# Performance work log

Hardware: AMD Instinct MI355X
Metric: run time of the kernel (lower is better)

## Reference

```python
import jax, jax.numpy as jnp
import numpy as np

B, N, IN_DIM, OUT_DIM, K = 64, 256, 512, 512, 8
DK = OUT_DIM // K  # per-kernel feature dim


def setup_inputs() -> dict:
    key = jax.random.key(0)
    k1, k2, k3, k4 = jax.random.split(key, 4)
    node_feats = jax.random.normal(k1, (B, N, IN_DIM), dtype=jnp.float32)
    adj = jax.random.uniform(k2, (B, K, N, N), dtype=jnp.float32)
    weight = jax.random.normal(k3, (IN_DIM, OUT_DIM), dtype=jnp.float32) * (1.0 / np.sqrt(IN_DIM))
    bias = jax.random.normal(k4, (OUT_DIM,), dtype=jnp.float32) * 0.01
    return {"node_feats": node_feats, "adj": adj, "weight": weight, "bias": bias}


def reference(node_feats, adj, weight, bias):
    # kernel linear + ReLU: (b, n, out_dim)
    h = jax.nn.relu(jnp.einsum('bni,io->bno', node_feats, weight) + bias)
    # split into kernel slots: (b, n, k, dk)
    h = h.reshape(B, N, K, DK)
    # graph.aggregate: per-kernel dense message passing over adjacency
    # out[b,n,k,d] = sum_m adj[b,k,n,m] * h[b,m,k,d]
    agg = jnp.einsum('bknm,bmkd->bnkd', adj, h)
    return agg.reshape(B, N, OUT_DIM)
```

## Files before the change

### kernel.cpp

```cpp
#include <hip/hip_runtime.h>
#include <hip/hip_bf16.h>


typedef __attribute__((ext_vector_type(8))) short short8;
typedef __attribute__((ext_vector_type(4))) float floatx4;

__device__ __forceinline__ unsigned short f2bf(float f) {
    union { float f; unsigned u; } v; v.f = f;
    unsigned r = v.u + 0x7FFFu + ((v.u >> 16) & 1u);
    return (unsigned short)(r >> 16);
}

__device__ __forceinline__ unsigned pk2bf(float a, float b) {
    union { __hip_bfloat162 h; unsigned u; } cv;
    cv.h = __float22bfloat162_rn(make_float2(a, b));
    return cv.u;
}

__global__ __launch_bounds__(256) void wt_kernel(const float* __restrict__ W,
                                                 unsigned short* __restrict__ Wt) {
    __shared__ unsigned short t_lds[64 * 66];
    const int tile = blockIdx.x;
    const int k0 = (tile >> 3) * 64;
    const int o0 = (tile & 7) * 64;
    const int t = threadIdx.x;
    const int c = t & 63;
    const int rb = t >> 6;
#pragma unroll
    for (int i = 0; i < 16; ++i) {
        int r = i * 4 + rb;
        t_lds[c * 66 + r] = f2bf(W[(size_t)(k0 + r) * 512 + o0 + c]);
    }
    __syncthreads();
#pragma unroll
    for (int i = 0; i < 16; ++i) {
        int o_r = i * 4 + rb;
        Wt[(size_t)(o0 + o_r) * 512 + k0 + c] = t_lds[o_r * 66 + c];
    }
}

__global__ __launch_bounds__(256) void gemm_relu_kernel(
    const float* __restrict__ X, const unsigned short* __restrict__ Wt,
    const float* __restrict__ bias, unsigned short* __restrict__ hT) {
    __shared__ unsigned short a_lds[128 * 40];
    __shared__ unsigned short b_lds[128 * 40];

    const int id = blockIdx.x;
    const int r8 = id & 7;
    const int yt = (id >> 3) & 3;
    const int q  = id >> 5;
    const int m_tile = r8 + 8 * q;
    const int m_base = m_tile * 128;
    const int o_base = yt * 128;

    const int tid = threadIdx.x;
    const int lane = tid & 63, wid = tid >> 6;
    const int wm = (wid & 1) * 64, wn = (wid >> 1) * 64;
    const int lrow = lane & 15, quad = lane >> 4;

    floatx4 acc[4][4];
    const floatx4 fzero = {0.f, 0.f, 0.f, 0.f};
#pragma unroll
    for (int i = 0; i < 4; ++i)
#pragma unroll
        for (int j = 0; j < 4; ++j) acc[i][j] = fzero;

    for (int kb = 0; kb < 16; ++kb) {
        const int k0 = kb * 32;
#pragma unroll
        for (int i = 0; i < 4; ++i) {
            int c4 = tid + i * 256;
            int rr = c4 >> 3;
            int cc = (c4 & 7) * 4;
            const float4 v = *(const float4*)(X + (size_t)(m_base + rr) * 512 + k0 + cc);
            unsigned p01 = pk2bf(v.x, v.y);
            unsigned p23 = pk2bf(v.z, v.w);
            unsigned* dst = (unsigned*)(a_lds + rr * 40 + cc);
            dst[0] = p01; dst[1] = p23;
        }
#pragma unroll
        for (int i = 0; i < 4; ++i) {
            int c4 = tid + i * 256;
            int rr = c4 >> 3;
            int cc = (c4 & 7) * 4;
            *(ushort4*)(b_lds + rr * 40 + cc) =
                *(const ushort4*)(Wt + (size_t)(o_base + rr) * 512 + k0 + cc);
        }
        __syncthreads();

        short8 af[4], bfr[4];
#pragma unroll
        for (int i = 0; i < 4; ++i)
            af[i] = *(const short8*)(a_lds + (wm + 16 * i + lrow) * 40 + quad * 8);
#pragma unroll
        for (int j = 0; j < 4; ++j)
            bfr[j] = *(const short8*)(b_lds + (wn + 16 * j + lrow) * 40 + quad * 8);
#pragma unroll
        for (int i = 0; i < 4; ++i)
#pragma unroll
            for (int j = 0; j < 4; ++j)
                acc[i][j] = __builtin_amdgcn_mfma_f32_16x16x32_bf16(af[i], bfr[j], acc[i][j], 0, 0, 0);
        __syncthreads();
    }

    const int b = m_tile >> 1;
    const int m_in_b = (m_tile & 1) * 128;
#pragma unroll
    for (int j = 0; j < 4; ++j) {
        int o = o_base + wn + 16 * j + lrow;
        float bv = bias[o];
        int ks = o >> 6, d = o & 63;
        unsigned short* dst = hT + ((size_t)(b * 8 + ks) * 64 + d) * 256;
#pragma unroll
        for (int i = 0; i < 4; ++i) {
            int m = m_in_b + wm + 16 * i + quad * 4;
            floatx4 c = acc[i][j];
            unsigned p01 = pk2bf(fmaxf(c.x + bv, 0.f), fmaxf(c.y + bv, 0.f));
            unsigned p23 = pk2bf(fmaxf(c.z + bv, 0.f), fmaxf(c.w + bv, 0.f));
            unsigned* d32 = (unsigned*)(dst + m);
            d32[0] = p01; d32[1] = p23;
        }
    }
}

__global__ __launch_bounds__(256) void agg_kernel(const float* __restrict__ adj,
                                                  const unsigned short* __restrict__ hT,
                                                  float* __restrict__ out) {
    const int id = blockIdx.x;
    const int r8 = id & 7;
    const int half = (id >> 3) & 1;
    const int q = id >> 4;
    const int bk = r8 + 8 * q;

    const int tid = threadIdx.x;
    const int lane = tid & 63, wid = tid >> 6;
    const int b = bk >> 3, ks = bk & 7;
    const int lrow = lane & 15, quad = lane >> 4;
    const int n0 = half * 128 + wid * 32;

    const float* A = adj + (size_t)bk * 65536;
    const unsigned short* Bh = hT + (size_t)bk * 16384;

    floatx4 acc[2][4];
    const floatx4 fzero = {0.f, 0.f, 0.f, 0.f};
#pragma unroll
    for (int i = 0; i < 2; ++i)
#pragma unroll
        for (int j = 0; j < 4; ++j) acc[i][j] = fzero;

    for (int mt = 0; mt < 8; ++mt) {
        const int m0 = mt * 32 + quad * 8;
        short8 af[2], bfr[4];
#pragma unroll
        for (int i = 0; i < 2; ++i) {
            const float* src = A + (size_t)(n0 + 16 * i + lrow) * 256 + m0;
            float4 v0 = *(const float4*)src;
            float4 v1 = *(const float4*)(src + 4);
            union { short8 s; unsigned u[4]; } t;
            t.u[0] = pk2bf(v0.x, v0.y);
            t.u[1] = pk2bf(v0.z, v0.w);
            t.u[2] = pk2bf(v1.x, v1.y);
            t.u[3] = pk2bf(v1.z, v1.w);
            af[i] = t.s;
        }
#pragma unroll
        for (int j = 0; j < 4; ++j)
            bfr[j] = *(const short8*)(Bh + (16 * j + lrow) * 256 + m0);
#pragma unroll
        for (int i = 0; i < 2; ++i)
#pragma unroll
            for (int j = 0; j < 4; ++j)
                acc[i][j] = __builtin_amdgcn_mfma_f32_16x16x32_bf16(af[i], bfr[j], acc[i][j], 0, 0, 0);
    }

#pragma unroll
    for (int i = 0; i < 2; ++i) {
#pragma unroll
        for (int j = 0; j < 4; ++j) {
            int n = n0 + 16 * i + quad * 4;
            int d = 16 * j + lrow;
            float* dst = out + ((size_t)b * 256 + n) * 512 + ks * 64 + d;
            floatx4 c = acc[i][j];
            dst[0 * 512] = c.x;
            dst[1 * 512] = c.y;
            dst[2 * 512] = c.z;
            dst[3 * 512] = c.w;
        }
    }
}

extern "C" void kernel_launch(void* const* d_in, const int* in_sizes, int n_in,
                              void* d_out, int out_size, void* d_ws, size_t ws_size,
                              hipStream_t stream) {
    const float* X    = (const float*)d_in[0];
    const float* adj  = (const float*)d_in[1];
    const float* W    = (const float*)d_in[2];
    const float* bias = (const float*)d_in[3];
    float* out = (float*)d_out;

    unsigned short* hT = (unsigned short*)d_ws;
    unsigned short* Wt = hT + (size_t)64 * 8 * 64 * 256;

    wt_kernel<<<64, 256, 0, stream>>>(W, Wt);
    gemm_relu_kernel<<<512, 256, 0, stream>>>(X, Wt, bias, hT);
    agg_kernel<<<1024, 256, 0, stream>>>(adj, hT, out);
}
```

Measured before the change: 255.2 us.

## Halve GEMM M-tile, double-buffer agg register fragments, add occupancy launch bounds

```diff
diff --git a/kernel.cpp b/kernel.cpp
--- a/kernel.cpp
+++ b/kernel.cpp
@@ -39,36 +39,36 @@
     }
 }
 
-__global__ __launch_bounds__(256) void gemm_relu_kernel(
+__global__ __launch_bounds__(256, 4) void gemm_relu_kernel(
     const float* __restrict__ X, const unsigned short* __restrict__ Wt,
     const float* __restrict__ bias, unsigned short* __restrict__ hT) {
-    __shared__ unsigned short a_lds[128 * 40];
+    __shared__ unsigned short a_lds[64 * 40];
     __shared__ unsigned short b_lds[128 * 40];
 
     const int id = blockIdx.x;
     const int r8 = id & 7;
-    const int yt = (id >> 3) & 3;
-    const int q  = id >> 5;
-    const int m_tile = r8 + 8 * q;
-    const int m_base = m_tile * 128;
-    const int o_base = yt * 128;
+    const int ot = (id >> 3) & 3;
+    const int g  = id >> 5;
+    const int m_tile = r8 + 8 * g;
+    const int m_base = m_tile * 64;
+    const int o_base = ot * 128;
 
     const int tid = threadIdx.x;
     const int lane = tid & 63, wid = tid >> 6;
-    const int wm = (wid & 1) * 64, wn = (wid >> 1) * 64;
+    const int wn = wid * 32;
     const int lrow = lane & 15, quad = lane >> 4;
 
-    floatx4 acc[4][4];
+    floatx4 acc[4][2];
     const floatx4 fzero = {0.f, 0.f, 0.f, 0.f};
 #pragma unroll
     for (int i = 0; i < 4; ++i)
 #pragma unroll
-        for (int j = 0; j < 4; ++j) acc[i][j] = fzero;
+        for (int j = 0; j < 2; ++j) acc[i][j] = fzero;
 
     for (int kb = 0; kb < 16; ++kb) {
         const int k0 = kb * 32;
 #pragma unroll
-        for (int i = 0; i < 4; ++i) {
+        for (int i = 0; i < 2; ++i) {
             int c4 = tid + i * 256;
             int rr = c4 >> 3;
             int cc = (c4 & 7) * 4;
@@ -88,32 +88,32 @@
         }
         __syncthreads();
 
-        short8 af[4], bfr[4];
+        short8 af[4], bfr[2];
 #pragma unroll
         for (int i = 0; i < 4; ++i)
-            af[i] = *(const short8*)(a_lds + (wm + 16 * i + lrow) * 40 + quad * 8);
-#pragma unroll
-        for (int j = 0; j < 4; ++j)
+            af[i] = *(const short8*)(a_lds + (16 * i + lrow) * 40 + quad * 8);
+#pragma unroll
+        for (int j = 0; j < 2; ++j)
             bfr[j] = *(const short8*)(b_lds + (wn + 16 * j + lrow) * 40 + quad * 8);
 #pragma unroll
         for (int i = 0; i < 4; ++i)
 #pragma unroll
-            for (int j = 0; j < 4; ++j)
+            for (int j = 0; j < 2; ++j)
                 acc[i][j] = __builtin_amdgcn_mfma_f32_16x16x32_bf16(af[i], bfr[j], acc[i][j], 0, 0, 0);
         __syncthreads();
     }
 
-    const int b = m_tile >> 1;
-    const int m_in_b = (m_tile & 1) * 128;
-#pragma unroll
-    for (int j = 0; j < 4; ++j) {
+    const int b = m_tile >> 2;
+    const int m_in_b0 = (m_tile & 3) * 64;
+#pragma unroll
+    for (int j = 0; j < 2; ++j) {
         int o = o_base + wn + 16 * j + lrow;
         float bv = bias[o];
         int ks = o >> 6, d = o & 63;
         unsigned short* dst = hT + ((size_t)(b * 8 + ks) * 64 + d) * 256;
 #pragma unroll
         for (int i = 0; i < 4; ++i) {
-            int m = m_in_b + wm + 16 * i + quad * 4;
+            int m = m_in_b0 + 16 * i + quad * 4;
             floatx4 c = acc[i][j];
             unsigned p01 = pk2bf(fmaxf(c.x + bv, 0.f), fmaxf(c.y + bv, 0.f));
             unsigned p23 = pk2bf(fmaxf(c.z + bv, 0.f), fmaxf(c.w + bv, 0.f));
@@ -123,9 +123,9 @@
     }
 }
 
-__global__ __launch_bounds__(256) void agg_kernel(const float* __restrict__ adj,
-                                                  const unsigned short* __restrict__ hT,
-                                                  float* __restrict__ out) {
+__global__ __launch_bounds__(256, 4) void agg_kernel(const float* __restrict__ adj,
+                                                     const unsigned short* __restrict__ hT,
+                                                     float* __restrict__ out) {
     const int id = blockIdx.x;
     const int r8 = id & 7;
     const int half = (id >> 3) & 1;
@@ -138,8 +138,9 @@
     const int lrow = lane & 15, quad = lane >> 4;
     const int n0 = half * 128 + wid * 32;
 
-    const float* A = adj + (size_t)bk * 65536;
-    const unsigned short* Bh = hT + (size_t)bk * 16384;
+    const float* A0 = adj + (size_t)bk * 65536 + (size_t)(n0 + lrow) * 256;
+    const float* A1 = A0 + 16 * 256;
+    const unsigned short* Bh = hT + (size_t)bk * 16384 + (size_t)lrow * 256;
 
     floatx4 acc[2][4];
     const floatx4 fzero = {0.f, 0.f, 0.f, 0.f};
@@ -148,14 +149,14 @@
 #pragma unroll
         for (int j = 0; j < 4; ++j) acc[i][j] = fzero;
 
-    for (int mt = 0; mt < 8; ++mt) {
-        const int m0 = mt * 32 + quad * 8;
-        short8 af[2], bfr[4];
+    short8 afc[2], bfc[4], afn[2], bfn[4];
+
+    auto load_frags = [&](int mo, short8* af, short8* bf) {
+        const float* srcs[2] = {A0 + mo, A1 + mo};
 #pragma unroll
         for (int i = 0; i < 2; ++i) {
-            const float* src = A + (size_t)(n0 + 16 * i + lrow) * 256 + m0;
-            float4 v0 = *(const float4*)src;
-            float4 v1 = *(const float4*)(src + 4);
+            float4 v0 = *(const float4*)(srcs[i]);
+            float4 v1 = *(const float4*)(srcs[i] + 4);
             union { short8 s; unsigned u[4]; } t;
             t.u[0] = pk2bf(v0.x, v0.y);
             t.u[1] = pk2bf(v0.z, v0.w);
@@ -165,12 +166,26 @@
         }
 #pragma unroll
         for (int j = 0; j < 4; ++j)
-            bfr[j] = *(const short8*)(Bh + (16 * j + lrow) * 256 + m0);
+            bf[j] = *(const short8*)(Bh + j * 16 * 256 + mo);
+    };
+
+    auto mfma8 = [&](short8* af, short8* bf) {
 #pragma unroll
         for (int i = 0; i < 2; ++i)
 #pragma unroll
             for (int j = 0; j < 4; ++j)
-                acc[i][j] = __builtin_amdgcn_mfma_f32_16x16x32_bf16(af[i], bfr[j], acc[i][j], 0, 0, 0);
+                acc[i][j] = __builtin_amdgcn_mfma_f32_16x16x32_bf16(af[i], bf[j], acc[i][j], 0, 0, 0);
+    };
+
+    int mo = quad * 8;
+    load_frags(mo, afc, bfc);
+#pragma unroll
+    for (int t = 0; t < 4; ++t) {
+        load_frags(mo + 32, afn, bfn);
+        mfma8(afc, bfc);
+        if (t < 3) load_frags(mo + 64, afc, bfc);
+        mfma8(afn, bfn);
+        mo += 64;
     }
 
 #pragma unroll
@@ -202,6 +217,6 @@
     unsigned short* Wt = hT + (size_t)64 * 8 * 64 * 256;
 
     wt_kernel<<<64, 256, 0, stream>>>(W, Wt);
-    gemm_relu_kernel<<<512, 256, 0, stream>>>(X, Wt, bias, hT);
+    gemm_relu_kernel<<<1024, 256, 0, stream>>>(X, Wt, bias, hT);
     agg_kernel<<<1024, 256, 0, stream>>>(adj, hT, out);
 }
```

New measurement: 262.2 us. 2.7% more time.

## Fuse linear+ReLU GEMM with per-kernel aggregation, keeping h in LDS

Applied to the files above, without the earlier changes.

```diff
diff --git a/kernel.cpp b/kernel.cpp
--- a/kernel.cpp
+++ b/kernel.cpp
@@ -39,121 +39,108 @@
     }
 }
 
-__global__ __launch_bounds__(256) void gemm_relu_kernel(
+__global__ __launch_bounds__(512, 4) void fused_kernel(
     const float* __restrict__ X, const unsigned short* __restrict__ Wt,
-    const float* __restrict__ bias, unsigned short* __restrict__ hT) {
-    __shared__ unsigned short a_lds[128 * 40];
-    __shared__ unsigned short b_lds[128 * 40];
+    const float* __restrict__ bias, const float* __restrict__ adj,
+    float* __restrict__ out) {
+    __shared__ union {
+        struct {
+            unsigned short a[256 * 40];
+            unsigned short w[64 * 40];
+        } s1;
+        unsigned short ht[64 * 264];
+    } lds;
 
     const int id = blockIdx.x;
-    const int r8 = id & 7;
-    const int yt = (id >> 3) & 3;
-    const int q  = id >> 5;
-    const int m_tile = r8 + 8 * q;
-    const int m_base = m_tile * 128;
-    const int o_base = yt * 128;
+    const int b = id & 63;
+    const int ks = id >> 6;
 
     const int tid = threadIdx.x;
-    const int lane = tid & 63, wid = tid >> 6;
-    const int wm = (wid & 1) * 64, wn = (wid >> 1) * 64;
+    const int lane = tid & 63, w = tid >> 6;
     const int lrow = lane & 15, quad = lane >> 4;
 
-    floatx4 acc[4][4];
+    const float* Xb = X + (size_t)b * 256 * 512;
+    const unsigned short* Wslice = Wt + (size_t)ks * 64 * 512;
+
+    floatx4 acc1[2][4];
     const floatx4 fzero = {0.f, 0.f, 0.f, 0.f};
 #pragma unroll
-    for (int i = 0; i < 4; ++i)
+    for (int i = 0; i < 2; ++i)
 #pragma unroll
-        for (int j = 0; j < 4; ++j) acc[i][j] = fzero;
+        for (int j = 0; j < 4; ++j) acc1[i][j] = fzero;
 
     for (int kb = 0; kb < 16; ++kb) {
         const int k0 = kb * 32;
 #pragma unroll
         for (int i = 0; i < 4; ++i) {
-            int c4 = tid + i * 256;
+            int c4 = tid + i * 512;
             int rr = c4 >> 3;
             int cc = (c4 & 7) * 4;
-            const float4 v = *(const float4*)(X + (size_t)(m_base + rr) * 512 + k0 + cc);
+            const float4 v = *(const float4*)(Xb + (size_t)rr * 512 + k0 + cc);
             unsigned p01 = pk2bf(v.x, v.y);
             unsigned p23 = pk2bf(v.z, v.w);
-            unsigned* dst = (unsigned*)(a_lds + rr * 40 + cc);
+            unsigned* dst = (unsigned*)(lds.s1.a + rr * 40 + cc);
             dst[0] = p01; dst[1] = p23;
         }
-#pragma unroll
-        for (int i = 0; i < 4; ++i) {
-            int c4 = tid + i * 256;
-            int rr = c4 >> 3;
-            int cc = (c4 & 7) * 4;
-            *(ushort4*)(b_lds + rr * 40 + cc) =
-                *(const ushort4*)(Wt + (size_t)(o_base + rr) * 512 + k0 + cc);
+        {
+            int rr = tid >> 3;
+            int cc = (tid & 7) * 4;
+            *(ushort4*)(lds.s1.w + rr * 40 + cc) =
+                *(const ushort4*)(Wslice + (size_t)rr * 512 + k0 + cc);
         }
         __syncthreads();
 
-        short8 af[4], bfr[4];
+        short8 af[2], bfr[4];
 #pragma unroll
-        for (int i = 0; i < 4; ++i)
-            af[i] = *(const short8*)(a_lds + (wm + 16 * i + lrow) * 40 + quad * 8);
+        for (int i = 0; i < 2; ++i)
+            af[i] = *(const short8*)(lds.s1.a + (w * 32 + 16 * i + lrow) * 40 + quad * 8);
 #pragma unroll
         for (int j = 0; j < 4; ++j)
-            bfr[j] = *(const short8*)(b_lds + (wn + 16 * j + lrow) * 40 + quad * 8);
+            bfr[j] = *(const short8*)(lds.s1.w + (16 * j + lrow) * 40 + quad * 8);
 #pragma unroll
-        for (int i = 0; i < 4; ++i)
+        for (int i = 0; i < 2; ++i)
 #pragma unroll
             for (int j = 0; j < 4; ++j)
-                acc[i][j] = __builtin_amdgcn_mfma_f32_16x16x32_bf16(af[i], bfr[j], acc[i][j], 0, 0, 0);
+                acc1[i][j] = __builtin_amdgcn_mfma_f32_16x16x32_bf16(af[i], bfr[j], acc1[i][j], 0, 0, 0);
         __syncthreads();
     }
 
-    const int b = m_tile >> 1;
-    const int m_in_b = (m_tile & 1) * 128;
 #pragma unroll
     for (int j = 0; j < 4; ++j) {
-        int o = o_base + wn + 16 * j + lrow;
-        float bv = bias[o];
-        int ks = o >> 6, d = o & 63;
-        unsigned short* dst = hT + ((size_t)(b * 8 + ks) * 64 + d) * 256;
+        int d = 16 * j + lrow;
+        float bv = bias[ks * 64 + d];
 #pragma unroll
-        for (int i = 0; i < 4; ++i) {
-            int m = m_in_b + wm + 16 * i + quad * 4;
-            floatx4 c = acc[i][j];
+        for (int i = 0; i < 2; ++i) {
+            int m = w * 32 + 16 * i + quad * 4;
+            floatx4 c = acc1[i][j];
             unsigned p01 = pk2bf(fmaxf(c.x + bv, 0.f), fmaxf(c.y + bv, 0.f));
             unsigned p23 = pk2bf(fmaxf(c.z + bv, 0.f), fmaxf(c.w + bv, 0.f));
-            unsigned* d32 = (unsigned*)(dst + m);
+            unsigned* d32 = (unsigned*)(lds.ht + d * 264 + m);
             d32[0] = p01; d32[1] = p23;
         }
     }
-}
+    __syncthreads();
 
-__global__ __launch_bounds__(256) void agg_kernel(const float* __restrict__ adj,
-                                                  const unsigned short* __restrict__ hT,
-                                                  float* __restrict__ out) {
-    const int id = blockIdx.x;
-    const int r8 = id & 7;
-    const int half = (id >> 3) & 1;
-    const int q = id >> 4;
-    const int bk = r8 + 8 * q;
+    const float* A = adj + (size_t)id * 65536;
+    const float* Abase = adj + ((size_t)(b * 8 + ks)) * 65536;
+    (void)A;
 
-    const int tid = threadIdx.x;
-    const int lane = tid & 63, wid = tid >> 6;
-    const int b = bk >> 3, ks = bk & 7;
-    const int lrow = lane & 15, quad = lane >> 4;
-    const int n0 = half * 128 + wid * 32;
-
-    const float* A = adj + (size_t)bk * 65536;
-    const unsigned short* Bh = hT + (size_t)bk * 16384;
-
-    floatx4 acc[2][4];
-    const floatx4 fzero = {0.f, 0.f, 0.f, 0.f};
+    floatx4 acc2[2][4];
 #pragma unroll
     for (int i = 0; i < 2; ++i)
 #pragma unroll
-        for (int j = 0; j < 4; ++j) acc[i][j] = fzero;
+        for (int j = 0; j < 4; ++j) acc2[i][j] = fzero;
 
+    const float* A0 = Abase + (size_t)(w * 32 + lrow) * 256;
+    const float* A1 = A0 + 16 * 256;
+
+#pragma unroll
     for (int mt = 0; mt < 8; ++mt) {
         const int m0 = mt * 32 + quad * 8;
         short8 af[2], bfr[4];
 #pragma unroll
         for (int i = 0; i < 2; ++i) {
-            const float* src = A + (size_t)(n0 + 16 * i + lrow) * 256 + m0;
+            const float* src = (i == 0 ? A0 : A1) + m0;
             float4 v0 = *(const float4*)src;
             float4 v1 = *(const float4*)(src + 4);
             union { short8 s; unsigned u[4]; } t;
@@ -165,22 +152,22 @@
         }
 #pragma unroll
         for (int j = 0; j < 4; ++j)
-            bfr[j] = *(const short8*)(Bh + (16 * j + lrow) * 256 + m0);
+            bfr[j] = *(const short8*)(lds.ht + (16 * j + lrow) * 264 + m0);
 #pragma unroll
         for (int i = 0; i < 2; ++i)
 #pragma unroll
             for (int j = 0; j < 4; ++j)
-                acc[i][j] = __builtin_amdgcn_mfma_f32_16x16x32_bf16(af[i], bfr[j], acc[i][j], 0, 0, 0);
+                acc2[i][j] = __builtin_amdgcn_mfma_f32_16x16x32_bf16(af[i], bfr[j], acc2[i][j], 0, 0, 0);
     }
 
 #pragma unroll
     for (int i = 0; i < 2; ++i) {
 #pragma unroll
         for (int j = 0; j < 4; ++j) {
-            int n = n0 + 16 * i + quad * 4;
+            int n = w * 32 + 16 * i + quad * 4;
             int d = 16 * j + lrow;
             float* dst = out + ((size_t)b * 256 + n) * 512 + ks * 64 + d;
-            floatx4 c = acc[i][j];
+            floatx4 c = acc2[i][j];
             dst[0 * 512] = c.x;
             dst[1 * 512] = c.y;
             dst[2 * 512] = c.z;
@@ -198,10 +185,8 @@
     const float* bias = (const float*)d_in[3];
     float* out = (float*)d_out;
 
-    unsigned short* hT = (unsigned short*)d_ws;
-    unsigned short* Wt = hT + (size_t)64 * 8 * 64 * 256;
+    unsigned short* Wt = (unsigned short*)d_ws;
 
     wt_kernel<<<64, 256, 0, stream>>>(W, Wt);
-    gemm_relu_kernel<<<512, 256, 0, stream>>>(X, Wt, bias, hT);
-    agg_kernel<<<1024, 256, 0, stream>>>(adj, hT, out);
+    fused_kernel<<<512, 512, 0, stream>>>(X, Wt, bias, adj, out);
 }
```

Result: no change. 250.3 us (-1.9%).
